# Optimization experiments

Hardware: AMD Instinct MI355X
Metric: run time of the kernel (lower is better)

## Reference

```python
import jax, jax.numpy as jnp
import numpy as np

B, T, D, H = 2, 2048, 1024, 16
Dh = D // H


def _rope(q, k):
    # q, k: (B, H, T, Dh), interleaved even/odd rotation
    t = q.shape[2]
    dh = q.shape[3]
    inv_freq = 1.0 / (10000.0 ** (jnp.arange(0, dh, 2, dtype=jnp.float32) / dh))
    pos = jnp.arange(t, dtype=jnp.float32)
    freqs = pos[:, None] * inv_freq[None, :]          # (T, Dh/2)
    sin = jnp.sin(freqs)[None, None]                  # (1,1,T,Dh/2)
    cos = jnp.cos(freqs)[None, None]

    def rot(x):
        xe, xo = x[..., ::2], x[..., 1::2]
        re = xe * cos - xo * sin
        ro = xe * sin + xo * cos
        return jnp.stack([re, ro], axis=-1).reshape(x.shape)

    return rot(q), rot(k)


def setup_inputs() -> dict:
    key = jax.random.key(0)
    k1, k2, k3 = jax.random.split(key, 3)
    s = 1.0 / np.sqrt(D)
    return {
        "x": jax.random.normal(k1, (B, T, D), dtype=jnp.float32),
        "w_qkv": jax.random.normal(k2, (3 * D, D), dtype=jnp.float32) * s,
        "b_qkv": jnp.zeros((3 * D,), dtype=jnp.float32),
        "w_out": jax.random.normal(k3, (D, D), dtype=jnp.float32) * s,
        "b_out": jnp.zeros((D,), dtype=jnp.float32),
    }


def reference(x, w_qkv, b_qkv, w_out, b_out):
    b, t, d = x.shape
    qkv = x @ w_qkv.T + b_qkv                         # (B,T,3D)
    q, k, v = jnp.split(qkv, 3, axis=-1)
    q = q.reshape(b, t, H, Dh).transpose(0, 2, 1, 3)  # (B,H,T,Dh)
    k = k.reshape(b, t, H, Dh).transpose(0, 2, 1, 3)
    v = v.reshape(b, t, H, Dh).transpose(0, 2, 1, 3)
    q, k = _rope(q, k)
    scores = jnp.einsum("bhtd,bhsd->bhts", q, k) / jnp.sqrt(jnp.float32(Dh))
    causal = jnp.tril(jnp.ones((t, t), dtype=bool))[None, None]
    scores = jnp.where(causal, scores, -jnp.inf)
    probs = jax.nn.softmax(scores, axis=-1)
    out = jnp.einsum("bhts,bhsd->bhtd", probs, v)     # (B,H,T,Dh)
    out = out.transpose(0, 2, 1, 3).reshape(b, t, d)
    return out @ w_out.T + b_out
```

## Files before the change

### kernel.cpp

```cpp
#include <hip/hip_runtime.h>
#include <hip/hip_bf16.h>
#include <math.h>
#include <type_traits>

#define B_ 2
#define T_ 2048
#define D_ 1024
#define H_ 16
#define DH_ 64

typedef __bf16 bf16_t;
typedef bf16_t bf16x8 __attribute__((ext_vector_type(8)));
typedef bf16_t bf16x4 __attribute__((ext_vector_type(4)));
typedef float f32x4 __attribute__((ext_vector_type(4)));

typedef __attribute__((address_space(1))) const void gas_void;
typedef __attribute__((address_space(3))) void las_void;

__device__ __forceinline__ void gld16(const void* g, void* l) {
    __builtin_amdgcn_global_load_lds((gas_void*)g, (las_void*)l, 16, 0, 0);
}

#define WAITALL() asm volatile("s_waitcnt vmcnt(0) lgkmcnt(0)" ::: "memory")
#define BARRIER() do { asm volatile("" ::: "memory"); __builtin_amdgcn_s_barrier(); asm volatile("" ::: "memory"); } while (0)

__global__ __launch_bounds__(256) void cvt3(const float* __restrict__ a,
                                            const float* __restrict__ b,
                                            const float* __restrict__ c,
                                            bf16_t* __restrict__ oa,
                                            bf16_t* __restrict__ ob,
                                            bf16_t* __restrict__ oc,
                                            float2* __restrict__ tab) {
    if (blockIdx.x >= 8192) {
        int j = (blockIdx.x - 8192) * 256 + threadIdx.x;
        int t = j >> 5, d2 = j & 31;
        float invf = exp2f(-(float)d2 * 0.4152410118609203f);
        float ang = (float)t * invf;
        float sn, cs;
        sincosf(ang, &sn, &cs);
        tab[j] = make_float2(cs, sn);
        return;
    }
    int i = blockIdx.x * 256 + threadIdx.x;
    const float* src; bf16_t* dst; int off;
    if (i < 1048576)      { src = a; dst = oa; off = i; }
    else if (i < 1835008) { src = b; dst = ob; off = i - 1048576; }
    else                  { src = c; dst = oc; off = i - 1835008; }
    float4 f = ((const float4*)src)[off];
    bf16x4 v = { (bf16_t)f.x, (bf16_t)f.y, (bf16_t)f.z, (bf16_t)f.w };
    ((bf16x4*)dst)[off] = v;
}

__global__ __launch_bounds__(512, 4) void gemmqkv(const bf16_t* __restrict__ A,
                                                  const bf16_t* __restrict__ Bw,
                                                  const float* __restrict__ bias,
                                                  const float2* __restrict__ tab,
                                                  bf16_t* __restrict__ q_out,
                                                  bf16_t* __restrict__ k_out,
                                                  bf16_t* __restrict__ vt_out) {
    __shared__ __align__(16) char smem[65536];

    int tid = threadIdx.x;
    int lane = tid & 63, wid = tid >> 6;
    int wm = wid >> 2, wn = wid & 3;
    int lr = lane & 15, lk = lane >> 4;

    int l = blockIdx.y * 12 + blockIdx.x;
    int u = (l & 7) * 48 + (l >> 3);
    int bx = u % 12;
    int by = u / 12;

    f32x4 acc[4][4];
    f32x4 z = {0.f, 0.f, 0.f, 0.f};
#pragma unroll
    for (int i = 0; i < 4; i++)
#pragma unroll
        for (int j = 0; j < 4; j++) acc[i][j] = z;

    int cb = (tid & 3) * 16;
    int rT = tid >> 2;
    int sw = cb ^ (((rT >> 1) & 3) << 4);
    const char* gAp  = (const char*)A  + ((size_t)(by * 128 + rT)) * 2048 + sw;
    const char* gBp0 = (const char*)Bw + ((size_t)(bx * 256 + rT)) * 2048 + sw;
    const char* gBp1 = (const char*)Bw + ((size_t)(bx * 256 + 128 + rT)) * 2048 + sw;

    auto stg = [&](int par, int kt) __attribute__((always_inline)) {
        char* base = smem + par * 24576;
        gld16(gAp  + kt * 64, base + tid * 16);
        gld16(gBp0 + kt * 64, base + 8192 + tid * 16);
        gld16(gBp1 + kt * 64, base + 16384 + tid * 16);
    };

    int offA[4], offB[4];
#pragma unroll
    for (int m = 0; m < 4; m++) {
        int row = wm * 64 + m * 16 + lr;
        offA[m] = row * 64 + ((lk * 16) ^ (((row >> 1) & 3) << 4));
    }
#pragma unroll
    for (int n = 0; n < 4; n++) {
        int row = wn * 64 + n * 16 + lr;
        offB[n] = 8192 + row * 64 + ((lk * 16) ^ (((row >> 1) & 3) << 4));
    }

    stg(0, 0);
    for (int kt = 0; kt < 32; ++kt) {
        const char* buf = smem + (kt & 1) * 24576;
        WAITALL();
        BARRIER();
        if (kt < 31) stg((kt + 1) & 1, kt + 1);
        bf16x8 Af[4], Bf[4];
#pragma unroll
        for (int m = 0; m < 4; m++) Af[m] = *(const bf16x8*)(buf + offA[m]);
#pragma unroll
        for (int n = 0; n < 4; n++) Bf[n] = *(const bf16x8*)(buf + offB[n]);
        __builtin_amdgcn_s_setprio(1);
#pragma unroll
        for (int m = 0; m < 4; m++)
#pragma unroll
            for (int n = 0; n < 4; n++)
                acc[m][n] = __builtin_amdgcn_mfma_f32_16x16x32_bf16(Af[m], Bf[n], acc[m][n], 0, 0, 0);
        __builtin_amdgcn_s_setprio(0);
    }
    WAITALL();
    BARRIER();

    int m_base = by * 128 + wm * 64;
    int n_base = bx * 256 + wn * 64;
    char* myL = smem + wid * 8192;
    int which = n_base >> 10;
    int h = (n_base & 1023) >> 6;
    int b = m_base >> 11, t0 = m_base & 2047;
    int bh = b * H_ + h;
    if (which == 2) {
#pragma unroll
        for (int m = 0; m < 4; m++)
#pragma unroll
            for (int n = 0; n < 4; n++) {
                int rd = n * 16 + lr;
                float bv = bias[n_base + rd];
#pragma unroll
                for (int j = 0; j < 4; j++) {
                    int ct = m * 16 + lk * 4 + j;
                    int ct2 = (ct & 32) | (((ct >> 2) & 3) << 3) | (((ct >> 4) & 1) << 2) | (ct & 3);
                    int addr = (rd * 128 + ct2 * 2) ^ ((rd & 7) << 4);
                    *(bf16_t*)(myL + addr) = (bf16_t)(acc[m][n][j] + bv);
                }
            }
#pragma unroll
        for (int it = 0; it < 8; it++) {
            int row = it * 8 + (lane >> 3);
            int byt = (lane & 7) * 16;
            bf16x8 val = *(const bf16x8*)(myL + ((row * 128 + byt) ^ ((row & 7) << 4)));
            *(bf16x8*)(vt_out + ((size_t)bh * DH_ + row) * T_ + t0 + (lane & 7) * 8) = val;
        }
    } else {
        bf16_t* dst = which ? k_out : q_out;
        float qscl = which ? 1.0f : 0.18033688011112042f;
#pragma unroll
        for (int m = 0; m < 4; m++)
#pragma unroll
            for (int n = 0; n < 4; n++) {
                int dh = n * 16 + lr;
                float bv = bias[n_base + dh];
                int dh2 = dh >> 1;
                bool even = (dh & 1) == 0;
#pragma unroll
                for (int j = 0; j < 4; j++) {
                    int rt = m * 16 + lk * 4 + j;
                    float v = acc[m][n][j] + bv;
                    float pp = __shfl_xor(v, 1);
                    float2 cs = tab[(t0 + rt) * 32 + dh2];
                    float r = even ? v * cs.x - pp * cs.y : v * cs.x + pp * cs.y;
                    r *= qscl;
                    int addr = (rt * 128 + dh * 2) ^ ((rt & 7) << 4);
                    *(bf16_t*)(myL + addr) = (bf16_t)r;
                }
            }
#pragma unroll
        for (int it = 0; it < 8; it++) {
            int row = it * 8 + (lane >> 3);
            int byt = (lane & 7) * 16;
            bf16x8 val = *(const bf16x8*)(myL + ((row * 128 + byt) ^ ((row & 7) << 4)));
            *(bf16x8*)(dst + ((size_t)bh * T_ + t0 + row) * DH_ + (lane & 7) * 8) = val;
        }
    }
}

__global__ __launch_bounds__(256) void gemm128o(const bf16_t* __restrict__ A,
                                                const bf16_t* __restrict__ Bw,
                                                const float* __restrict__ bias,
                                                float* __restrict__ f_out,
                                                int K, int N) {
    __shared__ __align__(16) char smem[49152];
    char* b0 = smem;
    char* b1 = smem + 16384;
    char* b2 = smem + 32768;

    int tid = threadIdx.x;
    int lane = tid & 63, wid = tid >> 6;
    int wr = wid >> 1, wc = wid & 1;
    int lr = lane & 15, lk = lane >> 4;

    int l = blockIdx.y * gridDim.x + blockIdx.x;
    int chunk = (gridDim.x * gridDim.y) >> 3;
    int u = (l & 7) * chunk + (l >> 3);
    int bx = u % gridDim.x;
    int by = u / gridDim.x;

    f32x4 acc[4][4];
    f32x4 z = {0.f, 0.f, 0.f, 0.f};
#pragma unroll
    for (int i = 0; i < 4; i++)
#pragma unroll
        for (int j = 0; j < 4; j++) acc[i][j] = z;

    const char* Ab = (const char*)(A + (size_t)by * 128 * K);
    const char* Bb = (const char*)(Bw + (size_t)bx * 128 * K);
    const int rowstride = K * 2;

    int p0 = tid * 16;
    int p1 = 4096 + tid * 16;
    int r0 = p0 >> 6, r1 = p1 >> 6;
    int cb0 = (p0 & 63) ^ (((r0 >> 1) & 3) << 4);
    int cb1 = (p1 & 63) ^ (((r1 >> 1) & 3) << 4);
    size_t gA0 = (size_t)r0 * rowstride + cb0;
    size_t gA1 = (size_t)r1 * rowstride + cb1;

    int oa[4], ob[4];
#pragma unroll
    for (int m = 0; m < 4; m++) {
        int row = wr * 64 + m * 16 + lr;
        oa[m] = row * 64 + ((lk * 16) ^ (((row >> 1) & 3) << 4));
    }
#pragma unroll
    for (int n = 0; n < 4; n++) {
        int row = wc * 64 + n * 16 + lr;
        ob[n] = row * 64 + ((lk * 16) ^ (((row >> 1) & 3) << 4));
    }

    auto stg = [&](char* buf, int ks) __attribute__((always_inline)) {
        const char* Ag = Ab + (size_t)ks * 64;
        const char* Bg = Bb + (size_t)ks * 64;
        gld16(Ag + gA0, buf + p0);
        gld16(Ag + gA1, buf + p1);
        gld16(Bg + gA0, buf + 8192 + p0);
        gld16(Bg + gA1, buf + 8192 + p1);
    };

    auto iterf = [&](auto vmc, char* buf, int ks, bool dostage) __attribute__((always_inline)) {
        constexpr int VM = decltype(vmc)::value;
        if constexpr (VM == 8)      asm volatile("s_waitcnt vmcnt(8)" ::: "memory");
        else if constexpr (VM == 4) asm volatile("s_waitcnt vmcnt(4)" ::: "memory");
        else                        asm volatile("s_waitcnt vmcnt(0)" ::: "memory");
        __builtin_amdgcn_s_barrier();
        asm volatile("" ::: "memory");
        bf16x8 Af[4], Bf[4];
#pragma unroll
        for (int m = 0; m < 4; m++) Af[m] = *(const bf16x8*)(buf + oa[m]);
#pragma unroll
        for (int n = 0; n < 4; n++) Bf[n] = *(const bf16x8*)(buf + 8192 + ob[n]);
#pragma unroll
        for (int m = 0; m < 4; m++)
#pragma unroll
            for (int n = 0; n < 4; n++)
                acc[m][n] = __builtin_amdgcn_mfma_f32_16x16x32_bf16(Af[m], Bf[n], acc[m][n], 0, 0, 0);
        asm volatile("" ::: "memory");
        __builtin_amdgcn_s_barrier();
        asm volatile("" ::: "memory");
        if (dostage) stg(buf, ks);
    };

    std::integral_constant<int, 8> c8;
    std::integral_constant<int, 4> c4;
    std::integral_constant<int, 0> c0;

    stg(b0, 0);
    stg(b1, 1);
    stg(b2, 2);
    for (int s = 0; s < 30; s += 3) {
        iterf(c8, b0, s + 3, s + 3 < 32);
        iterf(c8, b1, s + 4, s + 4 < 32);
        iterf(c8, b2, s + 5, s + 5 < 32);
    }
    iterf(c4, b0, 0, false);
    iterf(c0, b1, 0, false);

    int m_base = by * 128 + wr * 64;
    int n_base = bx * 128 + wc * 64;
#pragma unroll
    for (int m = 0; m < 4; m++) {
        int gm0 = m_base + m * 16 + lk * 4;
#pragma unroll
        for (int n = 0; n < 4; n++) {
            int nc = n_base + n * 16 + lr;
            float bv = bias[nc];
#pragma unroll
            for (int j = 0; j < 4; j++)
                f_out[(size_t)(gm0 + j) * N + nc] = acc[m][n][j] + bv;
        }
    }
}

__global__ __launch_bounds__(128, 2) void attn64p(const bf16_t* __restrict__ Q,
                                                  const bf16_t* __restrict__ K,
                                                  const bf16_t* __restrict__ Vt,
                                                  bf16_t* __restrict__ Ao) {
    __shared__ __align__(16) char smem[40960];

    int tid = threadIdx.x;
    int lane = tid & 63, wid = tid >> 6;
    int lr = lane & 15, lk = lane >> 4;
    int bidx = blockIdx.x;
    int xcd = bidx & 7;
    int bh = xcd * 4 + ((bidx >> 3) & 3);
    int qq = (bidx >> 5) & 7, tier = bidx >> 8;
    int qt = (tier == 0) ? qq : (tier == 1) ? 31 - qq : (tier == 2) ? 8 + qq : 23 - qq;
    int q0 = qt * 64;
    int qrelw = wid * 16 + lr;

    const bf16_t* QA = Q + ((size_t)bh * T_ + q0 + qrelw) * DH_;
    const bf16_t* QB = QA + 32 * DH_;
    bf16x8 qa0 = *(const bf16x8*)(QA + lk * 8);
    bf16x8 qa1 = *(const bf16x8*)(QA + 32 + lk * 8);
    bf16x8 qb0 = *(const bf16x8*)(QB + lk * 8);
    bf16x8 qb1 = *(const bf16x8*)(QB + 32 + lk * 8);

    f32x4 zz = {0.f, 0.f, 0.f, 0.f};
    f32x4 oa0[4], oa1[4];
#pragma unroll
    for (int dt = 0; dt < 4; dt++) { oa0[dt] = zz; oa1[dt] = zz; }
    float ls0 = 0.f, ls1 = 0.f;
    bf16x8 pA0, pA1, pB0, pB1;

    const char* Kbase = (const char*)(K + (size_t)bh * T_ * DH_);
    const char* Vbase = (const char*)(Vt + (size_t)bh * DH_ * T_);

    auto stage = [&](int s, char* Kd, char* Vd) __attribute__((always_inline)) {
        int kv0 = s * 64;
        const char* Kg = Kbase + (size_t)kv0 * 128;
#pragma unroll
        for (int c = 0; c < 4; c++) {
            int o = c * 2048 + tid * 16;
            int r = o >> 7;
            int g = o ^ ((r & 7) << 4);
            gld16(Kg + g, Kd + o);
            gld16(Vbase + (size_t)r * (T_ * 2) + kv0 * 2 + (g & 127), Vd + o);
        }
    };

    auto do_qk = [&](const char* Kc, bool dmask) __attribute__((always_inline)) {
#pragma unroll
        for (int kt = 0; kt < 4; kt++) {
            int row = kt * 16 + lr;
            int key = (row & 7) << 4;
            bf16x8 kf0 = *(const bf16x8*)(Kc + ((row * 128 + lk * 16) ^ key));
            bf16x8 kf1 = *(const bf16x8*)(Kc + ((row * 128 + 64 + lk * 16) ^ key));
            f32x4 s = zz;
            s = __builtin_amdgcn_mfma_f32_16x16x32_bf16(kf0, qa0, s, 0, 0, 0);
            s = __builtin_amdgcn_mfma_f32_16x16x32_bf16(kf1, qa1, s, 0, 0, 0);
#pragma unroll
            for (int j = 0; j < 4; j++) {
                float sv = s[j];
                if (dmask) {
                    int kv = kt * 16 + lk * 4 + j;
                    sv = (kv <= qrelw) ? sv : -__builtin_inff();
                }
                float e = exp2f(sv);
                ls0 += e;
                if (kt < 2) pA0[kt * 4 + j] = (bf16_t)e;
                else        pA1[(kt - 2) * 4 + j] = (bf16_t)e;
            }
            s = zz;
            s = __builtin_amdgcn_mfma_f32_16x16x32_bf16(kf0, qb0, s, 0, 0, 0);
            s = __builtin_amdgcn_mfma_f32_16x16x32_bf16(kf1, qb1, s, 0, 0, 0);
#pragma unroll
            for (int j = 0; j < 4; j++) {
                float sv = s[j];
                if (dmask) {
                    int kv = kt * 16 + lk * 4 + j;
                    sv = (kv <= 32 + qrelw) ? sv : -__builtin_inff();
                }
                float e = exp2f(sv);
                ls1 += e;
                if (kt < 2) pB0[kt * 4 + j] = (bf16_t)e;
                else        pB1[(kt - 2) * 4 + j] = (bf16_t)e;
            }
        }
    };

    auto do_pv = [&](const char* Vc) __attribute__((always_inline)) {
        __builtin_amdgcn_s_setprio(1);
#pragma unroll
        for (int dt = 0; dt < 4; dt++) {
            int row = dt * 16 + lr;
            int key = (row & 7) << 4;
            bf16x8 vf0 = *(const bf16x8*)(Vc + ((row * 128 + lk * 16) ^ key));
            bf16x8 vf1 = *(const bf16x8*)(Vc + ((row * 128 + 64 + lk * 16) ^ key));
            f32x4 a = oa0[dt];
            a = __builtin_amdgcn_mfma_f32_16x16x32_bf16(vf0, pA0, a, 0, 0, 0);
            a = __builtin_amdgcn_mfma_f32_16x16x32_bf16(vf1, pA1, a, 0, 0, 0);
            oa0[dt] = a;
            f32x4 b = oa1[dt];
            b = __builtin_amdgcn_mfma_f32_16x16x32_bf16(vf0, pB0, b, 0, 0, 0);
            b = __builtin_amdgcn_mfma_f32_16x16x32_bf16(vf1, pB1, b, 0, 0, 0);
            oa1[dt] = b;
        }
        __builtin_amdgcn_s_setprio(0);
    };

    char* Kcur = smem + 8192;
    char* Kalt = smem;
    char* Vprev = smem + 16384;
    char* Vcur  = smem + 24576;
    char* Vnext = smem + 32768;

    stage(0, Kalt, Vprev);
    if (qt > 0) {
        stage(1, Kcur, Vcur);
        asm volatile("s_waitcnt vmcnt(8)" ::: "memory");
    } else {
        WAITALL();
    }
    BARRIER();
    do_qk(Kalt, qt == 0);

    for (int s = 1; s <= qt; ++s) {
        WAITALL();
        BARRIER();
        if (s < qt) stage(s + 1, Kalt, Vnext);
        do_pv(Vprev);
        do_qk(Kcur, s == qt);
        char* t = Kcur; Kcur = Kalt; Kalt = t;
        t = Vprev; Vprev = Vcur; Vcur = Vnext; Vnext = t;
    }
    do_pv(Vprev);
    WAITALL();
    BARRIER();

    ls0 += __shfl_xor(ls0, 16); ls0 += __shfl_xor(ls0, 32);
    ls1 += __shfl_xor(ls1, 16); ls1 += __shfl_xor(ls1, 32);
    float ri0 = __builtin_amdgcn_rcpf(ls0);
    float ri1 = __builtin_amdgcn_rcpf(ls1);

    char* myL = smem + wid * 2048;
    int bb = bh >> 4, hh = bh & 15;
#pragma unroll
    for (int dt = 0; dt < 4; dt++)
#pragma unroll
        for (int j = 0; j < 4; j++) {
            int dh = dt * 16 + lk * 4 + j;
            int addr = (lr * 128 + dh * 2) ^ ((lr & 7) << 4);
            *(bf16_t*)(myL + addr) = (bf16_t)(oa0[dt][j] * ri0);
        }
#pragma unroll
    for (int it = 0; it < 2; it++) {
        int row = it * 8 + (lane >> 3);
        int byt = (lane & 7) * 16;
        bf16x8 val = *(const bf16x8*)(myL + ((row * 128 + byt) ^ ((row & 7) << 4)));
        int t = q0 + wid * 16 + row;
        *(bf16x8*)(Ao + ((size_t)bb * T_ + t) * D_ + hh * DH_ + (lane & 7) * 8) = val;
    }
#pragma unroll
    for (int dt = 0; dt < 4; dt++)
#pragma unroll
        for (int j = 0; j < 4; j++) {
            int dh = dt * 16 + lk * 4 + j;
            int addr = (lr * 128 + dh * 2) ^ ((lr & 7) << 4);
            *(bf16_t*)(myL + addr) = (bf16_t)(oa1[dt][j] * ri1);
        }
#pragma unroll
    for (int it = 0; it < 2; it++) {
        int row = it * 8 + (lane >> 3);
        int byt = (lane & 7) * 16;
        bf16x8 val = *(const bf16x8*)(myL + ((row * 128 + byt) ^ ((row & 7) << 4)));
        int t = q0 + 32 + wid * 16 + row;
        *(bf16x8*)(Ao + ((size_t)bb * T_ + t) * D_ + hh * DH_ + (lane & 7) * 8) = val;
    }
}

extern "C" void kernel_launch(void* const* d_in, const int* in_sizes, int n_in,
                              void* d_out, int out_size, void* d_ws, size_t ws_size,
                              hipStream_t stream) {
    const float* x     = (const float*)d_in[0];
    const float* w_qkv = (const float*)d_in[1];
    const float* b_qkv = (const float*)d_in[2];
    const float* w_out = (const float*)d_in[3];
    const float* b_out = (const float*)d_in[4];
    float* out = (float*)d_out;

    char* ws = (char*)d_ws;
    bf16_t* xb    = (bf16_t*)(ws);
    bf16_t* wqkvb = (bf16_t*)(ws + 8388608);
    bf16_t* wob   = (bf16_t*)(ws + 14680064);
    bf16_t* qb    = (bf16_t*)(ws + 16777216);
    bf16_t* kb    = (bf16_t*)(ws + 25165824);
    bf16_t* vtb   = (bf16_t*)(ws + 33554432);
    bf16_t* ab    = (bf16_t*)(ws + 41943040);
    float2* tab   = (float2*)(ws + 41943040);

    cvt3<<<8448, 256, 0, stream>>>(x, w_qkv, w_out, xb, wqkvb, wob, tab);

    gemmqkv<<<dim3(12, 32), 512, 0, stream>>>(xb, wqkvb, b_qkv, tab, qb, kb, vtb);
    attn64p<<<1024, 128, 0, stream>>>(qb, kb, vtb, ab);
    gemm128o<<<dim3(8, 32), 256, 0, stream>>>(ab, wob, b_out, out, 1024, 1024);
}
```

Measured before the change: 116.2 us.

## Use single-wave attention blocks processing 64 query rows per wave

Replaces the two-wave attention kernel with a one-wave-per-block kernel where each wave handles all four 16-row query groups, so each K/V fragment loaded from LDS feeds four MFMA groups instead of two. The staging drops to double-buffering with a simple load-then-compute loop, removes barriers and setprio, and reorders the query-tile schedule. This trades barrier and LDS-read overhead for fewer waves per CU, more registers per wave, and less overlap between loads and compute.

```diff
diff --git a/kernel.cpp b/kernel.cpp
--- a/kernel.cpp
+++ b/kernel.cpp
@@ -302,46 +302,51 @@
     }
 }
 
-__global__ __launch_bounds__(128, 2) void attn64p(const bf16_t* __restrict__ Q,
-                                                  const bf16_t* __restrict__ K,
-                                                  const bf16_t* __restrict__ Vt,
-                                                  bf16_t* __restrict__ Ao) {
-    __shared__ __align__(16) char smem[40960];
-
-    int tid = threadIdx.x;
-    int lane = tid & 63, wid = tid >> 6;
+__global__ __launch_bounds__(64, 2) void attnw(const bf16_t* __restrict__ Q,
+                                               const bf16_t* __restrict__ K,
+                                               const bf16_t* __restrict__ Vt,
+                                               bf16_t* __restrict__ Ao) {
+    __shared__ __align__(16) char smem[32768];
+
+    int lane = threadIdx.x;
     int lr = lane & 15, lk = lane >> 4;
     int bidx = blockIdx.x;
-    int xcd = bidx & 7;
-    int bh = xcd * 4 + ((bidx >> 3) & 3);
-    int qq = (bidx >> 5) & 7, tier = bidx >> 8;
-    int qt = (tier == 0) ? qq : (tier == 1) ? 31 - qq : (tier == 2) ? 8 + qq : 23 - qq;
+    int xcd = bidx & 7, idx = bidx >> 3;
+    int bh = xcd * 4 + (idx & 3);
+    int q5 = idx >> 2;
+    int qt = (q5 < 8) ? q5 : (q5 < 16) ? 23 - q5 : (q5 < 24) ? q5 : 55 - q5;
     int q0 = qt * 64;
-    int qrelw = wid * 16 + lr;
-
-    const bf16_t* QA = Q + ((size_t)bh * T_ + q0 + qrelw) * DH_;
-    const bf16_t* QB = QA + 32 * DH_;
-    bf16x8 qa0 = *(const bf16x8*)(QA + lk * 8);
-    bf16x8 qa1 = *(const bf16x8*)(QA + 32 + lk * 8);
-    bf16x8 qb0 = *(const bf16x8*)(QB + lk * 8);
-    bf16x8 qb1 = *(const bf16x8*)(QB + 32 + lk * 8);
+
+    const bf16_t* Qp = Q + ((size_t)bh * T_ + q0 + lr) * DH_;
+    bf16x8 qf0_0 = *(const bf16x8*)(Qp + 0 * 16 * DH_ + lk * 8);
+    bf16x8 qf1_0 = *(const bf16x8*)(Qp + 0 * 16 * DH_ + 32 + lk * 8);
+    bf16x8 qf0_1 = *(const bf16x8*)(Qp + 1 * 16 * DH_ + lk * 8);
+    bf16x8 qf1_1 = *(const bf16x8*)(Qp + 1 * 16 * DH_ + 32 + lk * 8);
+    bf16x8 qf0_2 = *(const bf16x8*)(Qp + 2 * 16 * DH_ + lk * 8);
+    bf16x8 qf1_2 = *(const bf16x8*)(Qp + 2 * 16 * DH_ + 32 + lk * 8);
+    bf16x8 qf0_3 = *(const bf16x8*)(Qp + 3 * 16 * DH_ + lk * 8);
+    bf16x8 qf1_3 = *(const bf16x8*)(Qp + 3 * 16 * DH_ + 32 + lk * 8);
 
     f32x4 zz = {0.f, 0.f, 0.f, 0.f};
-    f32x4 oa0[4], oa1[4];
-#pragma unroll
-    for (int dt = 0; dt < 4; dt++) { oa0[dt] = zz; oa1[dt] = zz; }
-    float ls0 = 0.f, ls1 = 0.f;
-    bf16x8 pA0, pA1, pB0, pB1;
+    f32x4 oacc[4][4];
+#pragma unroll
+    for (int g = 0; g < 4; g++)
+#pragma unroll
+        for (int dt = 0; dt < 4; dt++) oacc[g][dt] = zz;
+    float ls[4] = {0.f, 0.f, 0.f, 0.f};
+    bf16x8 pf[4][2];
 
     const char* Kbase = (const char*)(K + (size_t)bh * T_ * DH_);
     const char* Vbase = (const char*)(Vt + (size_t)bh * DH_ * T_);
 
-    auto stage = [&](int s, char* Kd, char* Vd) __attribute__((always_inline)) {
+    auto stage = [&](int s) __attribute__((always_inline)) {
         int kv0 = s * 64;
+        char* Kd = smem + (s & 1) * 8192;
+        char* Vd = smem + 16384 + (s & 1) * 8192;
         const char* Kg = Kbase + (size_t)kv0 * 128;
 #pragma unroll
-        for (int c = 0; c < 4; c++) {
-            int o = c * 2048 + tid * 16;
+        for (int c = 0; c < 8; c++) {
+            int o = c * 1024 + lane * 16;
             int r = o >> 7;
             int g = o ^ ((r & 7) << 4);
             gld16(Kg + g, Kd + o);
@@ -356,126 +361,79 @@
             int key = (row & 7) << 4;
             bf16x8 kf0 = *(const bf16x8*)(Kc + ((row * 128 + lk * 16) ^ key));
             bf16x8 kf1 = *(const bf16x8*)(Kc + ((row * 128 + 64 + lk * 16) ^ key));
-            f32x4 s = zz;
-            s = __builtin_amdgcn_mfma_f32_16x16x32_bf16(kf0, qa0, s, 0, 0, 0);
-            s = __builtin_amdgcn_mfma_f32_16x16x32_bf16(kf1, qa1, s, 0, 0, 0);
-#pragma unroll
-            for (int j = 0; j < 4; j++) {
-                float sv = s[j];
-                if (dmask) {
-                    int kv = kt * 16 + lk * 4 + j;
-                    sv = (kv <= qrelw) ? sv : -__builtin_inff();
+#pragma unroll
+            for (int g = 0; g < 4; g++) {
+                f32x4 s = zz;
+                bf16x8 qa = (g == 0) ? qf0_0 : (g == 1) ? qf0_1 : (g == 2) ? qf0_2 : qf0_3;
+                bf16x8 qb = (g == 0) ? qf1_0 : (g == 1) ? qf1_1 : (g == 2) ? qf1_2 : qf1_3;
+                s = __builtin_amdgcn_mfma_f32_16x16x32_bf16(kf0, qa, s, 0, 0, 0);
+                s = __builtin_amdgcn_mfma_f32_16x16x32_bf16(kf1, qb, s, 0, 0, 0);
+#pragma unroll
+                for (int j = 0; j < 4; j++) {
+                    float sv = s[j];
+                    if (dmask) {
+                        int kv = kt * 16 + lk * 4 + j;
+                        sv = (kv <= g * 16 + lr) ? sv : -__builtin_inff();
+                    }
+                    float e = exp2f(sv);
+                    ls[g] += e;
+                    pf[g][kt >> 1][(kt & 1) * 4 + j] = (bf16_t)e;
                 }
-                float e = exp2f(sv);
-                ls0 += e;
-                if (kt < 2) pA0[kt * 4 + j] = (bf16_t)e;
-                else        pA1[(kt - 2) * 4 + j] = (bf16_t)e;
             }
-            s = zz;
-            s = __builtin_amdgcn_mfma_f32_16x16x32_bf16(kf0, qb0, s, 0, 0, 0);
-            s = __builtin_amdgcn_mfma_f32_16x16x32_bf16(kf1, qb1, s, 0, 0, 0);
-#pragma unroll
-            for (int j = 0; j < 4; j++) {
-                float sv = s[j];
-                if (dmask) {
-                    int kv = kt * 16 + lk * 4 + j;
-                    sv = (kv <= 32 + qrelw) ? sv : -__builtin_inff();
-                }
-                float e = exp2f(sv);
-                ls1 += e;
-                if (kt < 2) pB0[kt * 4 + j] = (bf16_t)e;
-                else        pB1[(kt - 2) * 4 + j] = (bf16_t)e;
-            }
         }
     };
 
     auto do_pv = [&](const char* Vc) __attribute__((always_inline)) {
-        __builtin_amdgcn_s_setprio(1);
 #pragma unroll
         for (int dt = 0; dt < 4; dt++) {
             int row = dt * 16 + lr;
             int key = (row & 7) << 4;
             bf16x8 vf0 = *(const bf16x8*)(Vc + ((row * 128 + lk * 16) ^ key));
             bf16x8 vf1 = *(const bf16x8*)(Vc + ((row * 128 + 64 + lk * 16) ^ key));
-            f32x4 a = oa0[dt];
-            a = __builtin_amdgcn_mfma_f32_16x16x32_bf16(vf0, pA0, a, 0, 0, 0);
-            a = __builtin_amdgcn_mfma_f32_16x16x32_bf16(vf1, pA1, a, 0, 0, 0);
-            oa0[dt] = a;
-            f32x4 b = oa1[dt];
-            b = __builtin_amdgcn_mfma_f32_16x16x32_bf16(vf0, pB0, b, 0, 0, 0);
-            b = __builtin_amdgcn_mfma_f32_16x16x32_bf16(vf1, pB1, b, 0, 0, 0);
-            oa1[dt] = b;
-        }
-        __builtin_amdgcn_s_setprio(0);
-    };
-
-    char* Kcur = smem + 8192;
-    char* Kalt = smem;
-    char* Vprev = smem + 16384;
-    char* Vcur  = smem + 24576;
-    char* Vnext = smem + 32768;
-
-    stage(0, Kalt, Vprev);
-    if (qt > 0) {
-        stage(1, Kcur, Vcur);
-        asm volatile("s_waitcnt vmcnt(8)" ::: "memory");
-    } else {
+#pragma unroll
+            for (int g = 0; g < 4; g++) {
+                f32x4 o = oacc[g][dt];
+                o = __builtin_amdgcn_mfma_f32_16x16x32_bf16(vf0, pf[g][0], o, 0, 0, 0);
+                o = __builtin_amdgcn_mfma_f32_16x16x32_bf16(vf1, pf[g][1], o, 0, 0, 0);
+                oacc[g][dt] = o;
+            }
+        }
+    };
+
+    stage(0);
+    for (int s = 0; s <= qt; ++s) {
         WAITALL();
-    }
-    BARRIER();
-    do_qk(Kalt, qt == 0);
-
-    for (int s = 1; s <= qt; ++s) {
-        WAITALL();
-        BARRIER();
-        if (s < qt) stage(s + 1, Kalt, Vnext);
-        do_pv(Vprev);
-        do_qk(Kcur, s == qt);
-        char* t = Kcur; Kcur = Kalt; Kalt = t;
-        t = Vprev; Vprev = Vcur; Vcur = Vnext; Vnext = t;
-    }
-    do_pv(Vprev);
-    WAITALL();
-    BARRIER();
-
-    ls0 += __shfl_xor(ls0, 16); ls0 += __shfl_xor(ls0, 32);
-    ls1 += __shfl_xor(ls1, 16); ls1 += __shfl_xor(ls1, 32);
-    float ri0 = __builtin_amdgcn_rcpf(ls0);
-    float ri1 = __builtin_amdgcn_rcpf(ls1);
-
-    char* myL = smem + wid * 2048;
+        if (s < qt) stage(s + 1);
+        const char* Kc = smem + (s & 1) * 8192;
+        const char* Vc = smem + 16384 + (s & 1) * 8192;
+        do_qk(Kc, s == qt);
+        do_pv(Vc);
+    }
+    asm volatile("s_waitcnt lgkmcnt(0)" ::: "memory");
+
     int bb = bh >> 4, hh = bh & 15;
 #pragma unroll
-    for (int dt = 0; dt < 4; dt++)
-#pragma unroll
-        for (int j = 0; j < 4; j++) {
-            int dh = dt * 16 + lk * 4 + j;
-            int addr = (lr * 128 + dh * 2) ^ ((lr & 7) << 4);
-            *(bf16_t*)(myL + addr) = (bf16_t)(oa0[dt][j] * ri0);
-        }
-#pragma unroll
-    for (int it = 0; it < 2; it++) {
-        int row = it * 8 + (lane >> 3);
-        int byt = (lane & 7) * 16;
-        bf16x8 val = *(const bf16x8*)(myL + ((row * 128 + byt) ^ ((row & 7) << 4)));
-        int t = q0 + wid * 16 + row;
-        *(bf16x8*)(Ao + ((size_t)bb * T_ + t) * D_ + hh * DH_ + (lane & 7) * 8) = val;
-    }
-#pragma unroll
-    for (int dt = 0; dt < 4; dt++)
-#pragma unroll
-        for (int j = 0; j < 4; j++) {
-            int dh = dt * 16 + lk * 4 + j;
-            int addr = (lr * 128 + dh * 2) ^ ((lr & 7) << 4);
-            *(bf16_t*)(myL + addr) = (bf16_t)(oa1[dt][j] * ri1);
-        }
-#pragma unroll
-    for (int it = 0; it < 2; it++) {
-        int row = it * 8 + (lane >> 3);
-        int byt = (lane & 7) * 16;
-        bf16x8 val = *(const bf16x8*)(myL + ((row * 128 + byt) ^ ((row & 7) << 4)));
-        int t = q0 + 32 + wid * 16 + row;
-        *(bf16x8*)(Ao + ((size_t)bb * T_ + t) * D_ + hh * DH_ + (lane & 7) * 8) = val;
+    for (int g = 0; g < 4; g++) {
+        float l = ls[g];
+        l += __shfl_xor(l, 16);
+        l += __shfl_xor(l, 32);
+        float ri = __builtin_amdgcn_rcpf(l);
+#pragma unroll
+        for (int dt = 0; dt < 4; dt++)
+#pragma unroll
+            for (int j = 0; j < 4; j++) {
+                int dh = dt * 16 + lk * 4 + j;
+                int addr = (lr * 128 + dh * 2) ^ ((lr & 7) << 4);
+                *(bf16_t*)(smem + addr) = (bf16_t)(oacc[g][dt][j] * ri);
+            }
+#pragma unroll
+        for (int it = 0; it < 2; it++) {
+            int row = it * 8 + (lane >> 3);
+            int byt = (lane & 7) * 16;
+            bf16x8 val = *(const bf16x8*)(smem + ((row * 128 + byt) ^ ((row & 7) << 4)));
+            int t = q0 + g * 16 + row;
+            *(bf16x8*)(Ao + ((size_t)bb * T_ + t) * D_ + hh * DH_ + (lane & 7) * 8) = val;
+        }
     }
 }
 
@@ -502,6 +460,6 @@
     cvt3<<<8448, 256, 0, stream>>>(x, w_qkv, w_out, xb, wqkvb, wob, tab);
 
     gemmqkv<<<dim3(12, 32), 512, 0, stream>>>(xb, wqkvb, b_qkv, tab, qb, kb, vtb);
-    attn64p<<<1024, 128, 0, stream>>>(qb, kb, vtb, ab);
+    attnw<<<1024, 64, 0, stream>>>(qb, kb, vtb, ab);
     gemm128o<<<dim3(8, 32), 256, 0, stream>>>(ab, wob, b_out, out, 1024, 1024);
 }
```

Result: slower. 132.8 us (+14.3%).
